# Kernel optimization log

Measured on AMD Instinct MI355X. Metric: run time of the kernel, lower is better.

Reference implementation:

```python
import jax, jax.numpy as jnp
import numpy as np

N, B, C, H = 4096, 8, 512, 8
D = C // H
EPS = 1e-6


def setup_inputs() -> dict:
    key = jax.random.key(0)
    ks = jax.random.split(key, 6)
    scale = 0.02  # keep projections in a sane range so sigmoid isn't saturated
    return {
        "query": jax.random.normal(ks[0], (N, B, C), dtype=jnp.float32),
        "Wq": jax.random.normal(ks[1], (C, C), dtype=jnp.float32) * scale,
        "bq": jnp.zeros((C,), dtype=jnp.float32),
        "Wk": jax.random.normal(ks[2], (C, C), dtype=jnp.float32) * scale,
        "bk": jnp.zeros((C,), dtype=jnp.float32),
        "Wv": jax.random.normal(ks[3], (C, C), dtype=jnp.float32) * scale,
        "bv": jnp.zeros((C,), dtype=jnp.float32),
        "Wo": jax.random.normal(ks[4], (C, C), dtype=jnp.float32) * scale,
        "bo": jnp.zeros((C,), dtype=jnp.float32),
        "temperature": jnp.ones((1,), dtype=jnp.float32),
    }


def _dot(a, b):
    # a: (B,H,S,D), b: (B,H,D) -> (B,H,S)
    return jnp.einsum("bhsd,bhd->bhs", a, b)


def reference(query, Wq, bq, Wk, bk, Wv, bv, Wo, bo, temperature):
    n, b, c = query.shape  # self-attention: key = value = identity = query
    q = (query @ Wq + bq).reshape(n, b, H, D).transpose(1, 2, 0, 3)  # (B,H,N,D)
    k = (query @ Wk + bk).reshape(n, b, H, D).transpose(1, 2, 0, 3)  # (B,H,HW,D)
    v = (query @ Wv + bv).reshape(n, b, H, D).transpose(1, 2, 0, 3)  # (B,H,HW,D)
    q = jax.nn.sigmoid(q)  # kernel feature map
    k = jax.nn.sigmoid(k)

    hw = k.shape[2]
    # conservation normalizations (note: sum(a+eps, b) adds eps INSIDE the dot, matching torch)
    sink_incoming = 1.0 / (_dot(q + EPS, k.sum(axis=2) + EPS) + EPS)        # (B,H,N)
    source_outgoing = 1.0 / (_dot(k + EPS, q.sum(axis=2) + EPS) + EPS)      # (B,H,HW)
    conserved_sink = _dot(q + EPS, (k * source_outgoing[..., None]).sum(axis=2) + EPS) + EPS
    conserved_source = _dot(k + EPS, (q * sink_incoming[..., None]).sum(axis=2) + EPS) + EPS
    conserved_source = jnp.clip(conserved_source, -1.0, 1.0)

    sink_allocation = jax.nn.sigmoid(conserved_sink * (float(n) / float(hw)))  # (B,H,N)
    # torch does softmax over the key axis and multiplies by key.shape[2] == embed_dim C
    source_competition = jax.nn.softmax(conserved_source / temperature, axis=-1) * float(c)  # (B,H,HW)

    kv = jnp.einsum("bhsd,bhse->bhde", k, v * source_competition[..., None])  # (B,H,D,D)
    out_update = jnp.einsum("bhnd,bhde->bhne", q, kv)
    out_update = out_update * sink_incoming[..., None] * sink_allocation[..., None]  # (B,H,N,D)

    # faithful to torch: reshape (B,H,N,D) -> (B,N,C) directly (no head permute)
    out = out_update.reshape(b, n, c)
    out = out @ Wo + bo
    out = out.transpose(1, 0, 2)  # back to (N,B,C)
    return query + out  # identity residual (dropout is identity in eval)
```

## Files before the change

kernel.cpp:

```cpp
#include <hip/hip_runtime.h>
#include <stdint.h>

typedef unsigned short u16;
typedef unsigned int u32;

#define EPS 1e-6f
#define NSEQ 4096

typedef __bf16 bf16x8 __attribute__((ext_vector_type(8)));
typedef float f32x4 __attribute__((ext_vector_type(4)));

__device__ __forceinline__ float b2f(u16 u) {
  union { u32 i; float f; } x; x.i = ((u32)u) << 16; return x.f;
}
__device__ __forceinline__ u16 f2b(float f) {
  union { float f; u32 i; } x; x.f = f;
  u32 r = x.i + 0x7fffu + ((x.i >> 16) & 1u);
  return (u16)(r >> 16);
}
__device__ __forceinline__ u16 f2b_hw(float f) {
  union { __bf16 h; u16 u; } x; x.h = (__bf16)f; return x.u;
}
__device__ __forceinline__ void unpack8(const u16* p, float* o) {
  uint4 u = *(const uint4*)p;
  o[0]=b2f((u16)(u.x&0xffff)); o[1]=b2f((u16)(u.x>>16));
  o[2]=b2f((u16)(u.y&0xffff)); o[3]=b2f((u16)(u.y>>16));
  o[4]=b2f((u16)(u.z&0xffff)); o[5]=b2f((u16)(u.z>>16));
  o[6]=b2f((u16)(u.w&0xffff)); o[7]=b2f((u16)(u.w>>16));
}
__device__ __forceinline__ bool is_f32(const u16* tdisc) { return tdisc[0] != 0x3F80; }

__global__ void convert_small(const void* bq, const void* bk, const void* bv,
                              const void* bo, const void* temp,
                              float* __restrict__ bcat, float* __restrict__ scal) {
  bool f32 = is_f32((const u16*)temp);
  int t = threadIdx.x;
  for (int i = t; i < 512; i += 256) {
    bcat[i]      = f32 ? ((const float*)bq)[i] : b2f(((const u16*)bq)[i]);
    bcat[512+i]  = f32 ? ((const float*)bk)[i] : b2f(((const u16*)bk)[i]);
    bcat[1024+i] = f32 ? ((const float*)bv)[i] : b2f(((const u16*)bv)[i]);
    bcat[1536+i] = f32 ? ((const float*)bo)[i] : b2f(((const u16*)bo)[i]);
  }
  if (t == 0) scal[0] = f32 ? ((const float*)temp)[0] : b2f(((const u16*)temp)[0]);
}

__global__ void zero_small(float* __restrict__ qsum, float* __restrict__ ksum,
                           float* __restrict__ qsi, float* __restrict__ kso) {
  int i = blockIdx.x*256 + threadIdx.x;
  qsum[i]=0.f; ksum[i]=0.f; qsi[i]=0.f; kso[i]=0.f;
}

__global__ __launch_bounds__(256) void conv_q(const void* __restrict__ query,
                                              u16* __restrict__ Qbf,
                                              const u16* __restrict__ tdisc) {
  bool f32 = is_f32(tdisc);
  int i = (blockIdx.x*256 + threadIdx.x) * 8;
  if (f32) {
    const float* q = (const float*)query + i;
    float4 a = ((const float4*)q)[0];
    float4 b = ((const float4*)q)[1];
    union { u16 h[8]; uint4 u; } pk;
    pk.h[0]=f2b_hw(a.x); pk.h[1]=f2b_hw(a.y); pk.h[2]=f2b_hw(a.z); pk.h[3]=f2b_hw(a.w);
    pk.h[4]=f2b_hw(b.x); pk.h[5]=f2b_hw(b.y); pk.h[6]=f2b_hw(b.z); pk.h[7]=f2b_hw(b.w);
    *(uint4*)(Qbf + i) = pk.u;
  } else {
    *(uint4*)(Qbf + i) = *(const uint4*)((const u16*)query + i);
  }
}

__global__ void transpose_w(const void* Wq, const void* Wk,
                            const void* Wv, const void* Wo,
                            u16* __restrict__ Wt, const void* temp) {
  __shared__ u16 tile[32][33];
  bool f32 = is_f32((const u16*)temp);
  int wsel = blockIdx.z;
  const void* W = wsel==0?Wq:wsel==1?Wk:wsel==2?Wv:Wo;
  int x0 = blockIdx.x*32, y0 = blockIdx.y*32;
  int tx = threadIdx.x & 31, ty = threadIdx.x >> 5;
  #pragma unroll
  for (int i=0;i<32;i+=8) {
    int idx = (y0+ty+i)*512 + x0+tx;
    tile[ty+i][tx] = f32 ? f2b(((const float*)W)[idx]) : ((const u16*)W)[idx];
  }
  __syncthreads();
  #pragma unroll
  for (int i=0;i<32;i+=8)
    Wt[wsel*262144 + (x0+ty+i)*512 + (y0+tx)] = tile[tx][ty+i];
}

template<int MODE, bool GLOADA>
__global__ __launch_bounds__(256, 3) void gemm_kernel(
    const void* __restrict__ A, const u16* __restrict__ WtAll,
    const float* __restrict__ bcat, const void* __restrict__ query,
    u16* __restrict__ Qb, u16* __restrict__ Kb, u16* __restrict__ Vb,
    void* __restrict__ Outp, float* __restrict__ qsum, float* __restrict__ ksum,
    const u16* __restrict__ tdisc)
{
  __shared__ __align__(16) u16 smem[MODE==0 ? 17408 : 16384];
  bool f32 = is_f32(tdisc);
  int t = threadIdx.x;
  int lane = t & 63, w = t >> 6;
  int wr = w >> 1, wc = w & 1;
  int quad = lane >> 4, l15 = lane & 15;
  int orig = blockIdx.x;
  int wgid, y, bx;
  if (MODE==0) {
    wgid = (orig & 7) * 384 + (orig >> 3);
    y = wgid % 12; bx = wgid / 12;
  } else {
    wgid = (orig & 7) * 128 + (orig >> 3);
    y = wgid & 3;  bx = wgid >> 2;
  }
  int row0 = bx * 128;
  int wsel = (MODE==0) ? (y >> 2) : 3;
  int colw = (MODE==0) ? ((y & 3)*128) : (y*128);
  const u16* Bt = WtAll + wsel*262144 + colw*512;
  const u16* Abf = (const u16*)A;

  f32x4 zero4 = {0.f, 0.f, 0.f, 0.f};
  f32x4 acc[4][4];
  #pragma unroll
  for (int i=0;i<4;i++)
    #pragma unroll
    for (int j=0;j<4;j++) acc[i][j] = zero4;

  int sr = t >> 1;
  int scol = (t & 1) * 16;
  int aoff0 = sr*32 + scol;
  int aoff1 = sr*32 + scol + 8;
  int grow = t >> 2;
  int gcol = (t & 3) * 8;
  bool af32 = (MODE==0) && f32;

  float4 x0, x1, x2, x3;
  uint4 u0, u1;

  if (GLOADA) {
    __builtin_amdgcn_global_load_lds(
        (const __attribute__((address_space(1))) void*)(Abf + (size_t)(row0 + grow)*512 + gcol),
        (__attribute__((address_space(3))) void*)(smem + t*8), 16, 0, 0);
    __builtin_amdgcn_global_load_lds(
        (const __attribute__((address_space(1))) void*)(Abf + (size_t)(row0 + 64 + grow)*512 + gcol),
        (__attribute__((address_space(3))) void*)(smem + 2048 + t*8), 16, 0, 0);
  } else {
    if (af32) {
      const float* Af = (const float*)A + (row0+sr)*512 + scol;
      x0 = ((const float4*)Af)[0]; x1 = ((const float4*)Af)[1];
      x2 = ((const float4*)Af)[2]; x3 = ((const float4*)Af)[3];
    } else {
      const u16* Au = (const u16*)A + (row0+sr)*512 + scol;
      u0 = *(const uint4*)Au; u1 = *(const uint4*)(Au + 8);
    }
  }
  __builtin_amdgcn_global_load_lds(
      (const __attribute__((address_space(1))) void*)(Bt + (grow     )*512 + gcol),
      (__attribute__((address_space(3))) void*)(smem + 4096 + t*8), 16, 0, 0);
  __builtin_amdgcn_global_load_lds(
      (const __attribute__((address_space(1))) void*)(Bt + (grow + 64)*512 + gcol),
      (__attribute__((address_space(3))) void*)(smem + 4096 + 2048 + t*8), 16, 0, 0);
  if (!GLOADA) {
    union { u16 h[16]; uint4 u[2]; } ab;
    if (af32) {
      ab.h[0]=f2b_hw(x0.x);  ab.h[1]=f2b_hw(x0.y);  ab.h[2]=f2b_hw(x0.z);  ab.h[3]=f2b_hw(x0.w);
      ab.h[4]=f2b_hw(x1.x);  ab.h[5]=f2b_hw(x1.y);  ab.h[6]=f2b_hw(x1.z);  ab.h[7]=f2b_hw(x1.w);
      ab.h[8]=f2b_hw(x2.x);  ab.h[9]=f2b_hw(x2.y);  ab.h[10]=f2b_hw(x2.z); ab.h[11]=f2b_hw(x2.w);
      ab.h[12]=f2b_hw(x3.x); ab.h[13]=f2b_hw(x3.y); ab.h[14]=f2b_hw(x3.z); ab.h[15]=f2b_hw(x3.w);
    } else { ab.u[0] = u0; ab.u[1] = u1; }
    *(uint4*)(smem + aoff0) = ab.u[0];
    *(uint4*)(smem + aoff1) = ab.u[1];
  }
  __syncthreads();

  for (int tt = 0; tt < 16; ++tt) {
    const u16* bc = smem + ((tt & 1) ? 8192 : 0);
    u16* bn = smem + ((tt & 1) ? 0 : 8192);
    bool more = tt < 15;
    int k1 = (tt + 1) * 32;
    if (more) {
      if (GLOADA) {
        __builtin_amdgcn_global_load_lds(
            (const __attribute__((address_space(1))) void*)(Abf + (size_t)(row0 + grow)*512 + k1 + gcol),
            (__attribute__((address_space(3))) void*)(bn + t*8), 16, 0, 0);
        __builtin_amdgcn_global_load_lds(
            (const __attribute__((address_space(1))) void*)(Abf + (size_t)(row0 + 64 + grow)*512 + k1 + gcol),
            (__attribute__((address_space(3))) void*)(bn + 2048 + t*8), 16, 0, 0);
      } else {
        if (af32) {
          const float* Af = (const float*)A + (row0+sr)*512 + k1 + scol;
          x0 = ((const float4*)Af)[0]; x1 = ((const float4*)Af)[1];
          x2 = ((const float4*)Af)[2]; x3 = ((const float4*)Af)[3];
        } else {
          const u16* Au = (const u16*)A + (row0+sr)*512 + k1 + scol;
          u0 = *(const uint4*)Au; u1 = *(const uint4*)(Au + 8);
        }
      }
      __builtin_amdgcn_global_load_lds(
          (const __attribute__((address_space(1))) void*)(Bt + (grow     )*512 + k1 + gcol),
          (__attribute__((address_space(3))) void*)(bn + 4096 + t*8), 16, 0, 0);
      __builtin_amdgcn_global_load_lds(
          (const __attribute__((address_space(1))) void*)(Bt + (grow + 64)*512 + k1 + gcol),
          (__attribute__((address_space(3))) void*)(bn + 4096 + 2048 + t*8), 16, 0, 0);
    }
    bf16x8 af[4], bfr[4];
    #pragma unroll
    for (int mt=0;mt<4;mt++)
      af[mt] = *(const bf16x8*)(bc + (wr*64 + mt*16 + l15)*32 + quad*8);
    #pragma unroll
    for (int nt=0;nt<4;nt++)
      bfr[nt] = *(const bf16x8*)(bc + 4096 + (wc*64 + nt*16 + l15)*32 + quad*8);
    #pragma unroll
    for (int mt=0;mt<4;mt++)
      #pragma unroll
      for (int nt=0;nt<4;nt++)
        acc[mt][nt] = __builtin_amdgcn_mfma_f32_16x16x32_bf16(af[mt], bfr[nt], acc[mt][nt], 0, 0, 0);
    if (more) {
      if (!GLOADA) {
        union { u16 h[16]; uint4 u[2]; } ab;
        if (af32) {
          ab.h[0]=f2b_hw(x0.x);  ab.h[1]=f2b_hw(x0.y);  ab.h[2]=f2b_hw(x0.z);  ab.h[3]=f2b_hw(x0.w);
          ab.h[4]=f2b_hw(x1.x);  ab.h[5]=f2b_hw(x1.y);  ab.h[6]=f2b_hw(x1.z);  ab.h[7]=f2b_hw(x1.w);
          ab.h[8]=f2b_hw(x2.x);  ab.h[9]=f2b_hw(x2.y);  ab.h[10]=f2b_hw(x2.z); ab.h[11]=f2b_hw(x2.w);
          ab.h[12]=f2b_hw(x3.x); ab.h[13]=f2b_hw(x3.y); ab.h[14]=f2b_hw(x3.z); ab.h[15]=f2b_hw(x3.w);
        } else { ab.u[0] = u0; ab.u[1] = u1; }
        *(uint4*)(bn + aoff0) = ab.u[0];
        *(uint4*)(bn + aoff1) = ab.u[1];
      }
      __syncthreads();
    }
  }

  const float* bias = bcat + wsel*512;
  if (MODE==0) {
    u16* Cs = smem;
    __syncthreads();
    #pragma unroll
    for (int mt=0;mt<4;mt++) {
      #pragma unroll
      for (int nt=0;nt<4;nt++) {
        #pragma unroll
        for (int pp=0;pp<4;pp++) {
          int m = wr*64 + mt*16 + quad*4 + pp;
          int c = wc*64 + nt*16 + l15;
          float val = acc[mt][nt][pp] + bias[colw + c];
          if (wsel < 2) val = 1.f/(1.f+__expf(-val));
          Cs[m*136 + c] = f2b_hw(val);
        }
      }
    }
    __syncthreads();
    u16* dst = wsel==0?Qb:wsel==1?Kb:Vb;
    #pragma unroll
    for (int i=0;i<8;i++) {
      int idx = i*256 + t;
      int d8 = idx & 7, hl = (idx>>3)&1, m = idx>>4;
      int r = row0 + m;
      int bi = r & 7, nrow = r >> 3;
      int h = (colw >> 6) + hl;
      uint4 v = *(const uint4*)(Cs + m*136 + hl*64 + d8*8);
      *(uint4*)(dst + (((size_t)(bi*8+h))*NSEQ + nrow)*64 + d8*8) = v;
    }
    if (wsel < 2) {
      float* outp = wsel==0 ? qsum : ksum;
      #pragma unroll
      for (int i=0;i<4;i++) {
        int idx = i*256 + t;
        int c = idx & 127, bi = idx >> 7;
        float s = 0.f;
        #pragma unroll
        for (int j=0;j<16;j++) s += b2f(Cs[(j*8+bi)*136 + c]);
        int jj = colw + c; int h = jj>>6, d = jj&63;
        atomicAdd(&outp[(bi*8+h)*64 + d], s);
      }
    }
  } else {
    float* Cf = (float*)smem;
    const float* q32 = (const float*)query;
    const u16*  q16 = (const u16*)query;
    #pragma unroll
    for (int half=0; half<2; half++) {
      __syncthreads();
      if (wr == half) {
        #pragma unroll
        for (int mt=0;mt<4;mt++) {
          #pragma unroll
          for (int nt=0;nt<4;nt++) {
            #pragma unroll
            for (int pp=0;pp<4;pp++) {
              int m = mt*16 + quad*4 + pp;
              int cl = wc*64 + nt*16 + l15;
              Cf[m*128 + cl] = acc[mt][nt][pp] + bias[colw + cl];
            }
          }
        }
      }
      __syncthreads();
      #pragma unroll
      for (int i=0;i<8;i++) {
        int idx = i*256 + t;
        int m = idx >> 5, c4 = (idx & 31)*4;
        int off = (row0 + half*64 + m)*512 + colw + c4;
        float4 v = *(const float4*)&Cf[m*128 + c4];
        if (f32) {
          float4 res = *(const float4*)&q32[off];
          v.x += res.x; v.y += res.y; v.z += res.z; v.w += res.w;
          *(float4*)&((float*)Outp)[off] = v;
        } else {
          union { u16 h[4]; uint2 u; } o;
          o.h[0] = f2b(v.x + b2f(q16[off+0]));
          o.h[1] = f2b(v.y + b2f(q16[off+1]));
          o.h[2] = f2b(v.z + b2f(q16[off+2]));
          o.h[3] = f2b(v.w + b2f(q16[off+3]));
          *(uint2*)&((u16*)Outp)[off] = o.u;
        }
      }
    }
  }
}

__global__ __launch_bounds__(256) void rdcs_kernel(
    const u16* __restrict__ Q, const u16* __restrict__ K,
    const float* __restrict__ qsum, const float* __restrict__ ksum,
    float* __restrict__ si, float* __restrict__ so,
    float* __restrict__ qsi, float* __restrict__ kso) {
  int p = blockIdx.x & 63, chunk = blockIdx.x >> 6;
  int t = threadIdx.x, part = t & 7, rsub = t >> 3;
  int r = chunk*32 + rsub;
  float ks_e[8], qs_e[8];
  #pragma unroll
  for (int j=0;j<8;j++) {
    ks_e[j] = ksum[p*64 + part*8 + j] + EPS;
    qs_e[j] = qsum[p*64 + part*8 + j] + EPS;
  }
  float fq[8], fk[8];
  unpack8(Q + ((size_t)p*NSEQ + r)*64 + part*8, fq);
  unpack8(K + ((size_t)p*NSEQ + r)*64 + part*8, fk);
  float a1 = 0.f, a2 = 0.f;
  #pragma unroll
  for (int j=0;j<8;j++) { a1 += (fq[j]+EPS)*ks_e[j]; a2 += (fk[j]+EPS)*qs_e[j]; }
  #pragma unroll
  for (int s=1; s<8; s<<=1) { a1 += __shfl_xor(a1, s, 8); a2 += __shfl_xor(a2, s, 8); }
  float siv = 1.f/(a1+EPS), sov = 1.f/(a2+EPS);
  if (part == 0) { si[p*NSEQ+r] = siv; so[p*NSEQ+r] = sov; }
  __shared__ float red[32][64];
  #pragma unroll
  for (int j=0;j<8;j++) red[rsub][part*8+j] = fq[j]*siv;
  __syncthreads();
  if (t < 64) {
    float s = 0.f;
    #pragma unroll
    for (int g=0;g<32;g++) s += red[g][t];
    atomicAdd(&qsi[p*64+t], s);
  }
  __syncthreads();
  #pragma unroll
  for (int j=0;j<8;j++) red[rsub][part*8+j] = fk[j]*sov;
  __syncthreads();
  if (t < 64) {
    float s = 0.f;
    #pragma unroll
    for (int g=0;g<32;g++) s += red[g][t];
    atomicAdd(&kso[p*64+t], s);
  }
}

__global__ __launch_bounds__(256) void rowdot_kernel(const u16* __restrict__ Q, const u16* __restrict__ K,
                              const float* __restrict__ qvec, const float* __restrict__ kvec,
                              float* __restrict__ out1, float* __restrict__ out2) {
  int p = blockIdx.x & 63, chunk = blockIdx.x >> 6;
  int t = threadIdx.x;
  int part = t & 7, rsub = t >> 3;
  int r = chunk*32 + rsub;
  float kv_e[8], qv_e[8];
  #pragma unroll
  for (int j=0;j<8;j++) {
    kv_e[j] = kvec[p*64 + part*8 + j] + EPS;
    qv_e[j] = qvec[p*64 + part*8 + j] + EPS;
  }
  float f[8];
  float a1 = 0.f, a2 = 0.f;
  unpack8(Q + ((size_t)p*NSEQ + r)*64 + part*8, f);
  #pragma unroll
  for (int j=0;j<8;j++) a1 += (f[j]+EPS)*kv_e[j];
  unpack8(K + ((size_t)p*NSEQ + r)*64 + part*8, f);
  #pragma unroll
  for (int j=0;j<8;j++) a2 += (f[j]+EPS)*qv_e[j];
  #pragma unroll
  for (int s=4; s>0; s>>=1) {
    a1 += __shfl_down(a1, s, 8);
    a2 += __shfl_down(a2, s, 8);
  }
  if (part == 0) {
    a1 += EPS; a2 += EPS;
    out1[p*NSEQ+r] = 1.f/(1.f+__expf(-a1));
    out2[p*NSEQ+r] = fminf(fmaxf(a2, -1.f), 1.f);
  }
}

__global__ void softmax_kernel(const float* __restrict__ cs, float* __restrict__ sc,
                               float* __restrict__ kvbuf, const float* __restrict__ scal) {
  int p = blockIdx.x, t = threadIdx.x;
  for (int i = t; i < 4096; i += 256) kvbuf[p*4096 + i] = 0.f;
  float invT = 1.f / scal[0];
  float v[16];
  float m = -1e30f;
  #pragma unroll
  for (int i=0;i<16;i++) { v[i] = cs[p*NSEQ + i*256 + t] * invT; m = fmaxf(m, v[i]); }
  __shared__ float red[256];
  red[t] = m; __syncthreads();
  for (int sd=128; sd>0; sd>>=1) { if (t<sd) red[t]=fmaxf(red[t],red[t+sd]); __syncthreads(); }
  m = red[0]; __syncthreads();
  float s = 0.f;
  #pragma unroll
  for (int i=0;i<16;i++) { v[i] = __expf(v[i]-m); s += v[i]; }
  red[t] = s; __syncthreads();
  for (int sd=128; sd>0; sd>>=1) { if (t<sd) red[t]+=red[t+sd]; __syncthreads(); }
  float inv = 512.f / red[0];
  #pragma unroll
  for (int i=0;i<16;i++) sc[p*NSEQ + i*256 + t] = v[i]*inv;
}

__global__ __launch_bounds__(256) void kv_kernel(const u16* __restrict__ K, const u16* __restrict__ V,
                                                 const float* __restrict__ sc, float* __restrict__ kvbuf) {
  int p = blockIdx.x >> 4, chunk = blockIdx.x & 15;
  int t = threadIdx.x;
  __shared__ __align__(16) u16 ks[256*64];
  __shared__ __align__(16) u16 vs[256*64];
  const u16* Kp = K + ((size_t)p*NSEQ + chunk*256)*64;
  const u16* Vp = V + ((size_t)p*NSEQ + chunk*256)*64;
  const float* scp = sc + p*NSEQ + chunk*256;
  #pragma unroll
  for (int i=0;i<8;i++) {
    int l8 = i*256 + t;
    int eoff = l8*8;
    *(uint4*)&ks[eoff] = *(const uint4*)(Kp + eoff);
    float f[8]; unpack8(Vp + eoff, f);
    float wgt = scp[l8 >> 3];
    union { u16 h[8]; uint4 u; } pk;
    #pragma unroll
    for (int j=0;j<8;j++) pk.h[j] = f2b(f[j]*wgt);
    *(uint4*)&vs[eoff] = pk.u;
  }
  __syncthreads();
  int e0 = (t & 15)*4, d0 = (t >> 4)*4;
  float acc[4][4] = {};
  for (int s=0;s<256;s++) {
    float kf[4], vf[4];
    uint2 ku = *(const uint2*)&ks[s*64+d0];
    uint2 vu = *(const uint2*)&vs[s*64+e0];
    kf[0]=b2f((u16)(ku.x&0xffff)); kf[1]=b2f((u16)(ku.x>>16));
    kf[2]=b2f((u16)(ku.y&0xffff)); kf[3]=b2f((u16)(ku.y>>16));
    vf[0]=b2f((u16)(vu.x&0xffff)); vf[1]=b2f((u16)(vu.x>>16));
    vf[2]=b2f((u16)(vu.y&0xffff)); vf[3]=b2f((u16)(vu.y>>16));
    #pragma unroll
    for (int ii=0;ii<4;ii++)
      #pragma unroll
      for (int jj=0;jj<4;jj++)
        acc[ii][jj] += kf[ii]*vf[jj];
  }
  float* kvp = kvbuf + p*4096;
  #pragma unroll
  for (int ii=0;ii<4;ii++)
    #pragma unroll
    for (int jj=0;jj<4;jj++)
      atomicAdd(&kvp[(d0+ii)*64 + (e0+jj)], acc[ii][jj]);
}

__global__ __launch_bounds__(256, 3) void outupd_kernel(const u16* __restrict__ Q, const float* __restrict__ kvbuf,
                                                        const float* __restrict__ si, const float* __restrict__ sa,
                                                        u16* __restrict__ OU) {
  __shared__ __align__(16) u16 arena[16384];
  __shared__ float sisa[256];
  int p = blockIdx.x >> 4, chunk = blockIdx.x & 15;
  int t = threadIdx.x;
  int lane = t & 63, w = t >> 6;
  int quad = lane >> 4, l15 = lane & 15;
  int rbase = chunk*256;
  const float* kvp = kvbuf + p*4096;

  {
    int e = t & 63, dg = t >> 6;
    float v[16];
    #pragma unroll
    for (int j=0;j<16;j++) v[j] = kvp[(dg*16+j)*64 + e];
    #pragma unroll
    for (int sl=0; sl<2; sl++) {
      int s = dg*2 + sl;
      union { u16 h[8]; uint4 u; } pk;
      #pragma unroll
      for (int j=0;j<8;j++) pk.h[j] = f2b_hw(v[sl*8+j]);
      *(uint4*)&arena[e*64 + ((s ^ (e&7))<<3)] = pk.u;
    }
    int gr = p*NSEQ + rbase + t;
    sisa[t] = si[gr] * sa[gr];
  }
  __syncthreads();

  bf16x8 bfr[4][2];
  #pragma unroll
  for (int nt=0;nt<4;nt++) {
    int e = nt*16 + l15;
    #pragma unroll
    for (int kk=0;kk<2;kk++)
      bfr[nt][kk] = *(const bf16x8*)&arena[e*64 + (((kk*4+quad) ^ (e&7))<<3)];
  }

  f32x4 zero4 = {0.f,0.f,0.f,0.f};
  f32x4 acc[4][4];
  #pragma unroll
  for (int i=0;i<4;i++)
    #pragma unroll
    for (int j=0;j<4;j++) acc[i][j] = zero4;

  const u16* Qw = Q + ((size_t)(p*NSEQ + rbase + w*64))*64;
  #pragma unroll
  for (int mt=0;mt<4;mt++) {
    const u16* qa = Qw + (mt*16 + l15)*64;
    bf16x8 a0 = *(const bf16x8*)(qa + quad*8);
    bf16x8 a1 = *(const bf16x8*)(qa + 32 + quad*8);
    #pragma unroll
    for (int nt=0;nt<4;nt++) {
      acc[mt][nt] = __builtin_amdgcn_mfma_f32_16x16x32_bf16(a0, bfr[nt][0], acc[mt][nt], 0, 0, 0);
      acc[mt][nt] = __builtin_amdgcn_mfma_f32_16x16x32_bf16(a1, bfr[nt][1], acc[mt][nt], 0, 0, 0);
    }
  }

  __syncthreads();
  #pragma unroll
  for (int mt=0;mt<4;mt++) {
    #pragma unroll
    for (int nt=0;nt<4;nt++) {
      #pragma unroll
      for (int pp=0;pp<4;pp++) {
        int rl = w*64 + mt*16 + quad*4 + pp;
        arena[rl*64 + nt*16 + l15] = f2b_hw(acc[mt][nt][pp] * sisa[rl]);
      }
    }
  }
  __syncthreads();
  u16* dst = OU + ((size_t)(p*NSEQ + rbase + t))*64;
  #pragma unroll
  for (int i=0;i<8;i++) {
    int s = (i + t) & 7;
    *(uint4*)(dst + s*8) = *(const uint4*)&arena[t*64 + s*8];
  }
}

extern "C" void kernel_launch(void* const* d_in, const int* in_sizes, int n_in,
                              void* d_out, int out_size, void* d_ws, size_t ws_size,
                              hipStream_t stream) {
  const void* query = d_in[0];
  const void* Wq = d_in[1];
  const void* bq = d_in[2];
  const void* Wk = d_in[3];
  const void* bk = d_in[4];
  const void* Wv = d_in[5];
  const void* bv = d_in[6];
  const void* Wo = d_in[7];
  const void* bo = d_in[8];
  const void* temp = d_in[9];
  const u16* tdisc = (const u16*)temp;

  char* ws = (char*)d_ws;
  u16*   Vb   = (u16*)(ws + 0);
  u16*   OU   = Vb;
  u16*   Wt   = (u16*)(ws + 33554432);
  float* bcat = (float*)(ws + 35651584);
  float* scal = (float*)(ws + 35659776);
  float* qsum = (float*)(ws + 35667968);
  float* ksum = (float*)(ws + 35684352);
  float* qsi  = (float*)(ws + 35700736);
  float* kso  = (float*)(ws + 35717120);
  float* si   = (float*)(ws + 36700160);
  float* so   = (float*)(ws + 37748736);
  float* sa   = (float*)(ws + 38797312);
  float* cs   = (float*)(ws + 39845888);
  float* sc   = (float*)(ws + 40894464);
  float* kvb  = (float*)(ws + 41943040);
  u16*   Qbf  = (u16*)(ws + 44040192);
  bool bigws = ws_size >= (size_t)44040192 + 33554432;

  u16* Qb = (u16*)d_out;
  u16* Kb = (u16*)d_out + 16777216;

  convert_small<<<1, 256, 0, stream>>>(bq, bk, bv, bo, temp, bcat, scal);
  zero_small<<<16, 256, 0, stream>>>(qsum, ksum, qsi, kso);
  transpose_w<<<dim3(16,16,4), 256, 0, stream>>>(Wq, Wk, Wv, Wo, Wt, temp);
  if (bigws) {
    conv_q<<<8192, 256, 0, stream>>>(query, Qbf, tdisc);
    gemm_kernel<0, true><<<3072, 256, 0, stream>>>(Qbf, Wt, bcat, query,
                                                   Qb, Kb, Vb, nullptr, qsum, ksum, tdisc);
  } else {
    gemm_kernel<0, false><<<3072, 256, 0, stream>>>(query, Wt, bcat, query,
                                                    Qb, Kb, Vb, nullptr, qsum, ksum, tdisc);
  }
  rdcs_kernel<<<8192, 256, 0, stream>>>(Qb, Kb, qsum, ksum, si, so, qsi, kso);
  rowdot_kernel<<<8192, 256, 0, stream>>>(Qb, Kb, qsi, kso, sa, cs);
  softmax_kernel<<<64, 256, 0, stream>>>(cs, sc, kvb, scal);
  kv_kernel<<<1024, 256, 0, stream>>>(Kb, Vb, sc, kvb);
  outupd_kernel<<<1024, 256, 0, stream>>>(Qb, kvb, si, sa, OU);
  gemm_kernel<1, true><<<1024, 256, 0, stream>>>(OU, Wt, bcat, query,
                                                 nullptr, nullptr, nullptr, d_out,
                                                 qsum, ksum, tdisc);
}
```

Before: 369.3 us.

## Use MFMA for KV outer product, batch rows in rdcs, async K load to LDS

The kv_kernel's scalar 4x4 outer-product loop becomes bf16 MFMA 16x16x32 tiles, with each wave computing a 32x32 block of the 64x64 KV matrix. K is copied into LDS with global_load_lds instead of a register round-trip. rdcs_kernel now handles 128 rows per block instead of 32 and accumulates per thread before the shared reduction, cutting the block count and global atomics by a factor of four. The MFMA operands are gathered from LDS with strided 16-bit loads, which may cause bank conflicts and extra instructions.

```diff
diff --git a/kernel.cpp b/kernel.cpp
--- a/kernel.cpp
+++ b/kernel.cpp
@@ -324,26 +324,32 @@
     float* __restrict__ qsi, float* __restrict__ kso) {
   int p = blockIdx.x & 63, chunk = blockIdx.x >> 6;
   int t = threadIdx.x, part = t & 7, rsub = t >> 3;
-  int r = chunk*32 + rsub;
   float ks_e[8], qs_e[8];
   #pragma unroll
   for (int j=0;j<8;j++) {
     ks_e[j] = ksum[p*64 + part*8 + j] + EPS;
     qs_e[j] = qsum[p*64 + part*8 + j] + EPS;
   }
-  float fq[8], fk[8];
-  unpack8(Q + ((size_t)p*NSEQ + r)*64 + part*8, fq);
-  unpack8(K + ((size_t)p*NSEQ + r)*64 + part*8, fk);
-  float a1 = 0.f, a2 = 0.f;
-  #pragma unroll
-  for (int j=0;j<8;j++) { a1 += (fq[j]+EPS)*ks_e[j]; a2 += (fk[j]+EPS)*qs_e[j]; }
-  #pragma unroll
-  for (int s=1; s<8; s<<=1) { a1 += __shfl_xor(a1, s, 8); a2 += __shfl_xor(a2, s, 8); }
-  float siv = 1.f/(a1+EPS), sov = 1.f/(a2+EPS);
-  if (part == 0) { si[p*NSEQ+r] = siv; so[p*NSEQ+r] = sov; }
+  float qacc[8] = {0,0,0,0,0,0,0,0}, kacc[8] = {0,0,0,0,0,0,0,0};
+  #pragma unroll
+  for (int g=0; g<4; ++g) {
+    int r = chunk*128 + g*32 + rsub;
+    float fq[8], fk[8];
+    unpack8(Q + ((size_t)p*NSEQ + r)*64 + part*8, fq);
+    unpack8(K + ((size_t)p*NSEQ + r)*64 + part*8, fk);
+    float a1 = 0.f, a2 = 0.f;
+    #pragma unroll
+    for (int j=0;j<8;j++) { a1 += (fq[j]+EPS)*ks_e[j]; a2 += (fk[j]+EPS)*qs_e[j]; }
+    #pragma unroll
+    for (int s=1; s<8; s<<=1) { a1 += __shfl_xor(a1, s, 8); a2 += __shfl_xor(a2, s, 8); }
+    float siv = 1.f/(a1+EPS), sov = 1.f/(a2+EPS);
+    if (part == 0) { si[p*NSEQ+r] = siv; so[p*NSEQ+r] = sov; }
+    #pragma unroll
+    for (int j=0;j<8;j++) { qacc[j] += fq[j]*siv; kacc[j] += fk[j]*sov; }
+  }
   __shared__ float red[32][64];
   #pragma unroll
-  for (int j=0;j<8;j++) red[rsub][part*8+j] = fq[j]*siv;
+  for (int j=0;j<8;j++) red[rsub][part*8+j] = qacc[j];
   __syncthreads();
   if (t < 64) {
     float s = 0.f;
@@ -353,7 +359,7 @@
   }
   __syncthreads();
   #pragma unroll
-  for (int j=0;j<8;j++) red[rsub][part*8+j] = fk[j]*sov;
+  for (int j=0;j<8;j++) red[rsub][part*8+j] = kacc[j];
   __syncthreads();
   if (t < 64) {
     float s = 0.f;
@@ -423,6 +429,8 @@
                                                  const float* __restrict__ sc, float* __restrict__ kvbuf) {
   int p = blockIdx.x >> 4, chunk = blockIdx.x & 15;
   int t = threadIdx.x;
+  int lane = t & 63, w = t >> 6;
+  int quad = lane >> 4, l15 = lane & 15;
   __shared__ __align__(16) u16 ks[256*64];
   __shared__ __align__(16) u16 vs[256*64];
   const u16* Kp = K + ((size_t)p*NSEQ + chunk*256)*64;
@@ -432,7 +440,9 @@
   for (int i=0;i<8;i++) {
     int l8 = i*256 + t;
     int eoff = l8*8;
-    *(uint4*)&ks[eoff] = *(const uint4*)(Kp + eoff);
+    __builtin_amdgcn_global_load_lds(
+        (const __attribute__((address_space(1))) void*)(Kp + eoff),
+        (__attribute__((address_space(3))) void*)(ks + eoff), 16, 0, 0);
     float f[8]; unpack8(Vp + eoff, f);
     float wgt = scp[l8 >> 3];
     union { u16 h[8]; uint4 u; } pk;
@@ -441,28 +451,46 @@
     *(uint4*)&vs[eoff] = pk.u;
   }
   __syncthreads();
-  int e0 = (t & 15)*4, d0 = (t >> 4)*4;
-  float acc[4][4] = {};
-  for (int s=0;s<256;s++) {
-    float kf[4], vf[4];
-    uint2 ku = *(const uint2*)&ks[s*64+d0];
-    uint2 vu = *(const uint2*)&vs[s*64+e0];
-    kf[0]=b2f((u16)(ku.x&0xffff)); kf[1]=b2f((u16)(ku.x>>16));
-    kf[2]=b2f((u16)(ku.y&0xffff)); kf[3]=b2f((u16)(ku.y>>16));
-    vf[0]=b2f((u16)(vu.x&0xffff)); vf[1]=b2f((u16)(vu.x>>16));
-    vf[2]=b2f((u16)(vu.y&0xffff)); vf[3]=b2f((u16)(vu.y>>16));
-    #pragma unroll
-    for (int ii=0;ii<4;ii++)
-      #pragma unroll
-      for (int jj=0;jj<4;jj++)
-        acc[ii][jj] += kf[ii]*vf[jj];
+  int wr = w >> 1, wc = w & 1;
+  f32x4 zero4 = {0.f,0.f,0.f,0.f};
+  f32x4 acc[2][2];
+  acc[0][0]=zero4; acc[0][1]=zero4; acc[1][0]=zero4; acc[1][1]=zero4;
+  for (int ksb = 0; ksb < 8; ++ksb) {
+    int s0 = ksb*32 + quad*8;
+    bf16x8 a[2], b[2];
+    #pragma unroll
+    for (int dt=0; dt<2; ++dt) {
+      int d = wr*32 + dt*16 + l15;
+      union { u16 h[8]; bf16x8 v; } fa;
+      #pragma unroll
+      for (int j=0;j<8;j++) fa.h[j] = ks[(s0+j)*64 + d];
+      a[dt] = fa.v;
+    }
+    #pragma unroll
+    for (int et=0; et<2; ++et) {
+      int e = wc*32 + et*16 + l15;
+      union { u16 h[8]; bf16x8 v; } fb;
+      #pragma unroll
+      for (int j=0;j<8;j++) fb.h[j] = vs[(s0+j)*64 + e];
+      b[et] = fb.v;
+    }
+    #pragma unroll
+    for (int dt=0;dt<2;dt++)
+      #pragma unroll
+      for (int et=0;et<2;et++)
+        acc[dt][et] = __builtin_amdgcn_mfma_f32_16x16x32_bf16(a[dt], b[et], acc[dt][et], 0, 0, 0);
   }
   float* kvp = kvbuf + p*4096;
   #pragma unroll
-  for (int ii=0;ii<4;ii++)
-    #pragma unroll
-    for (int jj=0;jj<4;jj++)
-      atomicAdd(&kvp[(d0+ii)*64 + (e0+jj)], acc[ii][jj]);
+  for (int dt=0;dt<2;dt++)
+    #pragma unroll
+    for (int et=0;et<2;et++)
+      #pragma unroll
+      for (int pp=0;pp<4;pp++) {
+        int d = wr*32 + dt*16 + quad*4 + pp;
+        int e = wc*32 + et*16 + l15;
+        atomicAdd(&kvp[d*64 + e], acc[dt][et][pp]);
+      }
 }
 
 __global__ __launch_bounds__(256, 3) void outupd_kernel(const u16* __restrict__ Q, const float* __restrict__ kvbuf,
@@ -593,7 +621,7 @@
     gemm_kernel<0, false><<<3072, 256, 0, stream>>>(query, Wt, bcat, query,
                                                     Qb, Kb, Vb, nullptr, qsum, ksum, tdisc);
   }
-  rdcs_kernel<<<8192, 256, 0, stream>>>(Qb, Kb, qsum, ksum, si, so, qsi, kso);
+  rdcs_kernel<<<2048, 256, 0, stream>>>(Qb, Kb, qsum, ksum, si, so, qsi, kso);
   rowdot_kernel<<<8192, 256, 0, stream>>>(Qb, Kb, qsi, kso, sa, cs);
   softmax_kernel<<<64, 256, 0, stream>>>(cs, sc, kvb, scal);
   kv_kernel<<<1024, 256, 0, stream>>>(Kb, Vb, sc, kvb);
```

After: 313.9 us. 15.0% less time.
